# Kernel optimization log

Measured on AMD Instinct MI355X. Metric: run time of the kernel, lower is better.

The kernel has to match this reference:

```python
import jax, jax.numpy as jnp
import numpy as np

B, N, F = 2048, 65536, 128
NUM_K = 3
NUM_LABELS = 10
EXPONENT = 2.0


def setup_inputs() -> dict:
    key = jax.random.key(0)
    k1, k2, k3 = jax.random.split(key, 3)
    # positive inputs: tf.pow with a float exponent NaNs on negative bases
    x_input = jax.random.uniform(k1, (B, F), dtype=jnp.float32)
    train_inputs = jax.random.uniform(k2, (N, F), dtype=jnp.float32)
    train_labels = jax.random.randint(k3, (N,), 0, NUM_LABELS, dtype=jnp.int32)
    features = jnp.ones((F,), dtype=jnp.float32)  # abe_features, ones init
    return {
        "x_input": x_input,
        "train_inputs": train_inputs,
        "train_labels": train_labels,
        "features": features,
    }


def reference(x_input, train_inputs, train_labels, features):
    # weighted_inputs = features * train_inputs
    w = features[None, :] * train_inputs  # [N, F]

    # Minkowsky distance (faithful to the TF graph):
    # (sum(x^p) + sum(w^p))^(1/p) - 2 * x @ w^T
    left = jnp.sum(x_input ** EXPONENT, axis=1)[:, None]   # [B, 1]
    right = jnp.sum(w ** EXPONENT, axis=1)[None, :]        # [1, N]
    distance = (left + right) ** (1.0 / EXPONENT) - 2.0 * (x_input @ w.T)  # [B, N]

    # top-k nearest neighbors via top_k of negated distances
    values, indices = jax.lax.top_k(-distance, NUM_K)      # [B, K]

    # gather neighbor labels and average (tf.reduce_mean on int = floor div)
    labels = train_labels[indices]                          # [B, K] int32
    outputs = jnp.sum(labels, axis=1) // NUM_K              # [B] int32
    one_hot = jax.nn.one_hot(outputs, NUM_LABELS, dtype=jnp.float32)  # [B, NUM_LABELS]

    return (one_hot, values, indices, labels)
```

## Files before the change

### kernel.cpp

```cpp
#include <hip/hip_runtime.h>
#include <hip/hip_bf16.h>
#include <cstdint>
#include <cstddef>

typedef short bf16x8 __attribute__((ext_vector_type(8)));
typedef float f32x4 __attribute__((ext_vector_type(4)));

namespace {
constexpr int kB = 2048;
constexpr int kN = 65536;
constexpr int kF = 128;
constexpr int kLabels = 10;
constexpr int kIMax = 0x7fffffff;

constexpr int BM = 256;
constexpr int BN = 256;
constexpr int SLICE = 2048;
constexpr int NTILES = SLICE / BN;
constexpr int NCH = 12;
constexpr int NCHT = NTILES * NCH;
constexpr int NSUB = kN / 32;
constexpr float kMargin = 0.05f;
}

#define TOP3_INSERT(dd, ii, D0, I0, D1, I1, D2, I2)                              \
  do {                                                                           \
    float _d = (dd); int _i = (ii);                                              \
    if (_d < (D0) || (_d == (D0) && _i < (I0))) {                                \
      (D2) = (D1); (I2) = (I1); (D1) = (D0); (I1) = (I0); (D0) = _d; (I0) = _i;  \
    } else if (_d < (D1) || (_d == (D1) && _i < (I1))) {                         \
      (D2) = (D1); (I2) = (I1); (D1) = _d; (I1) = _i;                            \
    } else if (_d < (D2) || (_d == (D2) && _i < (I2))) {                         \
      (D2) = _d; (I2) = _i;                                                      \
    }                                                                            \
  } while (0)

__device__ inline unsigned short f2bf(float a) {
  __hip_bfloat16 h = __float2bfloat16(a);
  return __builtin_bit_cast(unsigned short, h);
}
__device__ inline float bf2f(unsigned short u) {
  return __bfloat162float(__builtin_bit_cast(__hip_bfloat16, u));
}

__device__ inline void gload_lds16(const void* g, void* l) {
  __builtin_amdgcn_global_load_lds(
      (const __attribute__((address_space(1))) void*)g,
      (__attribute__((address_space(3))) void*)l, 16, 0, 0);
}

__global__ __launch_bounds__(256) void pack_sumsq_kernel(
    const float* __restrict__ x, const float* __restrict__ train,
    const float* __restrict__ features, unsigned short* __restrict__ Ap,
    unsigned short* __restrict__ Bp, float* __restrict__ left,
    float* __restrict__ right) {
  const int wid = (int)((blockIdx.x * 256 + threadIdx.x) >> 6);
  const int lane = threadIdx.x & 63;
  if (wid >= kB + kN) return;
  const float2 fv = reinterpret_cast<const float2*>(features)[lane];
  const float* src;
  unsigned short* dst;
  float pm0, pm1, sm0, sm1;
  if (wid < kB) {
    src = x + (size_t)wid * kF;
    dst = Ap + (size_t)wid * 256;
    pm0 = fv.x; pm1 = fv.y;
    sm0 = 1.0f; sm1 = 1.0f;
  } else {
    src = train + (size_t)(wid - kB) * kF;
    dst = Bp + (size_t)(wid - kB) * 256;
    pm0 = 1.0f; pm1 = 1.0f;
    sm0 = fv.x; sm1 = fv.y;
  }
  const float2 v = reinterpret_cast<const float2*>(src)[lane];
  const float pa = v.x * pm0, pb = v.y * pm1;
  const float sa = v.x * sm0, sb = v.y * sm1;
  const unsigned short ha = f2bf(pa), hb = f2bf(pb);
  const unsigned short la = f2bf(pa - bf2f(ha)), lb = f2bf(pb - bf2f(hb));
  reinterpret_cast<unsigned int*>(dst)[lane] = (unsigned int)ha | ((unsigned int)hb << 16);
  reinterpret_cast<unsigned int*>(dst + 128)[lane] = (unsigned int)la | ((unsigned int)lb << 16);
  float s = sa * sa + sb * sb;
  #pragma unroll
  for (int m = 1; m <= 32; m <<= 1) s += __shfl_xor(s, m);
  if (lane == 0) {
    if (wid < kB) left[wid] = s;
    else right[wid - kB] = s;
  }
}

__global__ __launch_bounds__(512, 2) void knn_main_kernel(
    const unsigned short* __restrict__ Ap, const unsigned short* __restrict__ Bp,
    const float* __restrict__ left, const float* __restrict__ right,
    float* __restrict__ minbuf) {
  __shared__ alignas(16) unsigned short lsA[4][BM * 32];
  __shared__ alignas(16) unsigned short lsB[4][BN * 32];
  __shared__ alignas(16) float lsR[SLICE];

  const int slice = blockIdx.x;
  const int mb = blockIdx.y;
  const int row0 = mb * BM;
  const int col0 = slice * SLICE;
  const int t = threadIdx.x;
  const int lane = t & 63;
  const int wm = (t >> 6) >> 1;
  const int wn = (t >> 6) & 1;

  reinterpret_cast<float4*>(lsR)[t] =
      reinterpret_cast<const float4*>(right + col0)[t];

  float lrow[4][4];
  #pragma unroll
  for (int mf = 0; mf < 4; ++mf)
    #pragma unroll
    for (int rg = 0; rg < 4; ++rg)
      lrow[mf][rg] = left[row0 + wm * 64 + mf * 16 + (lane >> 4) * 4 + rg];

  const int rA = t >> 2;
  const int p = t & 3;
  size_t gbaseA[2], gbaseB[2];
  int ldsoff[2];
  #pragma unroll
  for (int i = 0; i < 2; ++i) {
    const int r = i * 128 + rA;
    const int ps = p ^ ((r >> 1) & 3);
    gbaseA[i] = (size_t)(row0 + r) * 512 + (size_t)ps * 16;
    gbaseB[i] = (size_t)(col0 + r) * 512 + (size_t)ps * 16;
    ldsoff[i] = i * 8192 + t * 16;
  }

  int offA[4], offB[8];
  #pragma unroll
  for (int mf = 0; mf < 4; ++mf) {
    const int rl = wm * 64 + mf * 16 + (lane & 15);
    offA[mf] = rl * 64 + (((lane >> 4) ^ ((rl >> 1) & 3)) * 16);
  }
  #pragma unroll
  for (int nf = 0; nf < 8; ++nf) {
    const int cl = wn * 128 + nf * 16 + (lane & 15);
    offB[nf] = cl * 64 + (((lane >> 4) ^ ((cl >> 1) & 3)) * 16);
  }

  const char* ApB = (const char*)Ap;
  const char* BpB = (const char*)Bp;

  auto stage = [&](int buf, int c, int nt) {
    const int skA = (c < 4) ? c * 32 : ((c < 8) ? 128 + (c - 4) * 32 : (c - 8) * 32);
    const int skB = (c < 4) ? c * 32 : ((c < 8) ? (c - 4) * 32 : 128 + (c - 8) * 32);
    char* lA = (char*)&lsA[buf][0];
    char* lB = (char*)&lsB[buf][0];
    #pragma unroll
    for (int i = 0; i < 2; ++i) {
      gload_lds16(ApB + gbaseA[i] + (size_t)skA * 2, lA + ldsoff[i]);
      gload_lds16(BpB + gbaseB[i] + (size_t)nt * 131072 + (size_t)skB * 2, lB + ldsoff[i]);
    }
  };

  const bool writer = ((lane >> 2) & 3) == (lane >> 4);

  asm volatile("s_waitcnt vmcnt(0) lgkmcnt(0)" ::: "memory");
  __syncthreads();

  int pn = 0, pc = 0;
  #pragma unroll
  for (int i = 0; i < 3; ++i) {
    stage(i, pc, pn);
    if (++pc == NCH) { pc = 0; ++pn; }
  }

  int g = 0;
  for (int nt = 0; nt < NTILES; ++nt) {
    f32x4 acc[4][8];
    #pragma unroll
    for (int mf = 0; mf < 4; ++mf)
      #pragma unroll
      for (int nf = 0; nf < 8; ++nf)
        acc[mf][nf] = (f32x4){0.f, 0.f, 0.f, 0.f};

    for (int c = 0; c < NCH; ++c, ++g) {
      if (g + 3 < NCHT) {
        stage((g + 3) & 3, pc, pn);
        if (++pc == NCH) { pc = 0; ++pn; }
      }
      {
        const int rem = NCHT - 1 - g;
        if (rem >= 3)      asm volatile("s_waitcnt vmcnt(12)" ::: "memory");
        else if (rem == 2) asm volatile("s_waitcnt vmcnt(8)" ::: "memory");
        else if (rem == 1) asm volatile("s_waitcnt vmcnt(4)" ::: "memory");
        else               asm volatile("s_waitcnt vmcnt(0)" ::: "memory");
      }
      __builtin_amdgcn_s_barrier();
      asm volatile("" ::: "memory");

      const char* lA = (const char*)&lsA[g & 3][0];
      const char* lB = (const char*)&lsB[g & 3][0];
      bf16x8 a[4], b[8];
      #pragma unroll
      for (int mf = 0; mf < 4; ++mf)
        a[mf] = *reinterpret_cast<const bf16x8*>(lA + offA[mf]);
      #pragma unroll
      for (int nf = 0; nf < 8; ++nf)
        b[nf] = *reinterpret_cast<const bf16x8*>(lB + offB[nf]);
      asm volatile("s_waitcnt lgkmcnt(0)" ::: "memory");
      __builtin_amdgcn_sched_barrier(0);
      __builtin_amdgcn_s_setprio(1);
      #pragma unroll
      for (int mf = 0; mf < 4; ++mf)
        #pragma unroll
        for (int nf = 0; nf < 8; ++nf)
          acc[mf][nf] = __builtin_amdgcn_mfma_f32_16x16x32_bf16(
              a[mf], b[nf], acc[mf][nf], 0, 0, 0);
      __builtin_amdgcn_s_setprio(0);
      __builtin_amdgcn_s_barrier();
      asm volatile("" ::: "memory");
    }

    float rj[8];
    #pragma unroll
    for (int nf = 0; nf < 8; ++nf)
      rj[nf] = lsR[nt * 256 + wn * 128 + nf * 16 + (lane & 15)];
    const int subbase = slice * 64 + nt * 8 + wn * 4;
    #pragma unroll
    for (int mf = 0; mf < 4; ++mf) {
      #pragma unroll
      for (int rg = 0; rg < 4; ++rg) {
        const float l = lrow[mf][rg];
        float m0, m1, m2, m3;
        #pragma unroll
        for (int nfp = 0; nfp < 4; ++nfp) {
          float da = sqrtf(l + rj[2 * nfp]) - 2.0f * acc[mf][2 * nfp][rg];
          float db = sqrtf(l + rj[2 * nfp + 1]) - 2.0f * acc[mf][2 * nfp + 1][rg];
          float mm = fminf(da, db);
          mm = fminf(mm, __shfl_xor(mm, 1));
          mm = fminf(mm, __shfl_xor(mm, 2));
          mm = fminf(mm, __shfl_xor(mm, 4));
          mm = fminf(mm, __shfl_xor(mm, 8));
          if (nfp == 0) m0 = mm; else if (nfp == 1) m1 = mm;
          else if (nfp == 2) m2 = mm; else m3 = mm;
        }
        if (writer) {
          const int row = row0 + wm * 64 + mf * 16 + (lane >> 4) * 4 + rg;
          const int nfp = lane & 3;
          const float vv = (nfp == 0) ? m0 : (nfp == 1) ? m1 : (nfp == 2) ? m2 : m3;
          minbuf[(size_t)row * NSUB + subbase + nfp] = vv;
        }
      }
    }
  }
}

__global__ __launch_bounds__(256) void select_rescore_kernel(
    const float* __restrict__ x, const float* __restrict__ train,
    const float* __restrict__ features, const float* __restrict__ left,
    const float* __restrict__ right, const int* __restrict__ labels,
    const float* __restrict__ minbuf, float* __restrict__ out) {
  __shared__ float Xs[4][kF];
  const int t = threadIdx.x;
  if (t < 128) {
    const int rr = t >> 5, q = t & 31;
    float4 xv = reinterpret_cast<const float4*>(
        x + (size_t)(blockIdx.x * 4 + rr) * kF)[q];
    const float4 f = reinterpret_cast<const float4*>(features)[q];
    xv.x *= f.x; xv.y *= f.y; xv.z *= f.z; xv.w *= f.w;
    reinterpret_cast<float4*>(&Xs[rr][0])[q] = xv;
  }
  __syncthreads();
  const int wave = t >> 6, lane = t & 63;
  const int row = blockIdx.x * 4 + wave;
  const float lr = left[row];
  const float* mrow = minbuf + (size_t)row * NSUB;

  float v0 = __builtin_inff(), v1 = v0, v2 = v0;
  #pragma unroll 4
  for (int i = 0; i < NSUB / 64; ++i) {
    const float m = mrow[i * 64 + lane];
    if (m < v0) { v2 = v1; v1 = v0; v0 = m; }
    else if (m < v1) { v2 = v1; v1 = m; }
    else if (m < v2) { v2 = m; }
  }
  #pragma unroll
  for (int msk = 1; msk <= 32; msk <<= 1) {
    const float e0 = __shfl_xor(v0, msk), e1 = __shfl_xor(v1, msk), e2 = __shfl_xor(v2, msk);
    if (e0 < v0) { v2 = v1; v1 = v0; v0 = e0; } else if (e0 < v1) { v2 = v1; v1 = e0; } else if (e0 < v2) v2 = e0;
    if (e1 < v0) { v2 = v1; v1 = v0; v0 = e1; } else if (e1 < v1) { v2 = v1; v1 = e1; } else if (e1 < v2) v2 = e1;
    if (e2 < v0) { v2 = v1; v1 = v0; v0 = e2; } else if (e2 < v1) { v2 = v1; v1 = e2; } else if (e2 < v2) v2 = e2;
  }
  const float tau = v2 + kMargin;

  float d0 = __builtin_inff(), d1 = d0, d2 = d0;
  int i0 = kIMax, i1 = kIMax, i2 = kIMax;
  for (int base = 0; base < NSUB; base += 64) {
    const float m = mrow[base + lane];
    unsigned long long msk = __ballot(m <= tau);
    while (msk) {
      const int bpos = __builtin_ctzll(msk);
      msk &= msk - 1;
      const int sub = base + bpos;
      if (lane < 32) {
        const int j = sub * 32 + lane;
        const float4* wp = reinterpret_cast<const float4*>(train + (size_t)j * kF);
        float acc = 0.f;
        #pragma unroll 8
        for (int kq = 0; kq < 32; ++kq) {
          const float4 w4 = wp[kq];
          const float4 x4 = reinterpret_cast<const float4*>(&Xs[wave][0])[kq];
          acc = fmaf(x4.w, w4.w, fmaf(x4.z, w4.z, fmaf(x4.y, w4.y, fmaf(x4.x, w4.x, acc))));
        }
        const float d = sqrtf(lr + right[j]) - 2.0f * acc;
        TOP3_INSERT(d, j, d0, i0, d1, i1, d2, i2);
      }
    }
  }
  #pragma unroll
  for (int msk = 1; msk <= 32; msk <<= 1) {
    const float e0 = __shfl_xor(d0, msk), e1 = __shfl_xor(d1, msk), e2 = __shfl_xor(d2, msk);
    const int f0 = __shfl_xor(i0, msk), f1 = __shfl_xor(i1, msk), f2 = __shfl_xor(i2, msk);
    TOP3_INSERT(e0, f0, d0, i0, d1, i1, d2, i2);
    TOP3_INSERT(e1, f1, d0, i0, d1, i1, d2, i2);
    TOP3_INSERT(e2, f2, d0, i0, d1, i1, d2, i2);
  }
  if (lane == 0) {
    const int l0 = labels[i0], l1 = labels[i1], l2 = labels[i2];
    const int o = (l0 + l1 + l2) / 3;
    float* one_hot = out;
    float* values = out + (size_t)kB * kLabels;
    float* indices = values + (size_t)kB * 3;
    float* labs = indices + (size_t)kB * 3;
    #pragma unroll
    for (int c = 0; c < kLabels; ++c)
      one_hot[(size_t)row * kLabels + c] = (c == o) ? 1.0f : 0.0f;
    values[row * 3 + 0] = -d0; values[row * 3 + 1] = -d1; values[row * 3 + 2] = -d2;
    indices[row * 3 + 0] = (float)i0; indices[row * 3 + 1] = (float)i1; indices[row * 3 + 2] = (float)i2;
    labs[row * 3 + 0] = (float)l0; labs[row * 3 + 1] = (float)l1; labs[row * 3 + 2] = (float)l2;
  }
}

extern "C" void kernel_launch(void* const* d_in, const int* in_sizes, int n_in,
                              void* d_out, int out_size, void* d_ws, size_t ws_size,
                              hipStream_t stream) {
  const float* x = (const float*)d_in[0];
  const float* train = (const float*)d_in[1];
  const int* labels = (const int*)d_in[2];
  const float* features = (const float*)d_in[3];
  float* out = (float*)d_out;

  char* ws = (char*)d_ws;
  unsigned short* Bp = (unsigned short*)ws;
  unsigned short* Ap = (unsigned short*)(ws + 33554432);
  float* left = (float*)(ws + 34603008);
  float* right = (float*)(ws + 34611200);
  float* minbuf = (float*)(ws + 34873344);

  pack_sumsq_kernel<<<((kB + kN) * 64 + 255) / 256, 256, 0, stream>>>(
      x, train, features, Ap, Bp, left, right);
  knn_main_kernel<<<dim3(32, 8), 512, 0, stream>>>(Ap, Bp, left, right, minbuf);
  select_rescore_kernel<<<kB / 4, 256, 0, stream>>>(
      x, train, features, left, right, labels, minbuf, out);
}
```

Measured before the change: 337.7 us.

## Regroup min-bins to cut shuffles in epilogue and drop explicit LDS wait

Each 32-candidate bin is redefined as a strided set of columns: a lane-group's 4 columns across all 8 n-fragments. Most of the min reduction then happens in registers, with only two xor-shuffles instead of sixteen per row. The rescore kernel's index mapping is changed to match the new bin membership. The explicit lgkmcnt wait and sched_barrier before the MFMAs are also removed, letting the compiler interleave LDS reads with MFMA issue. In exchange, the rescore kernel's global reads of training rows become less contiguous.

```diff
diff --git a/kernel.cpp b/kernel.cpp
--- a/kernel.cpp
+++ b/kernel.cpp
@@ -155,8 +155,6 @@
     }
   };
 
-  const bool writer = ((lane >> 2) & 3) == (lane >> 4);
-
   asm volatile("s_waitcnt vmcnt(0) lgkmcnt(0)" ::: "memory");
   __syncthreads();
 
@@ -166,6 +164,8 @@
     stage(i, pc, pn);
     if (++pc == NCH) { pc = 0; ++pn; }
   }
+
+  const bool bwriter = (lane & 3) == 0;
 
   int g = 0;
   for (int nt = 0; nt < NTILES; ++nt) {
@@ -200,8 +200,6 @@
       #pragma unroll
       for (int nf = 0; nf < 8; ++nf)
         b[nf] = *reinterpret_cast<const bf16x8*>(lB + offB[nf]);
-      asm volatile("s_waitcnt lgkmcnt(0)" ::: "memory");
-      __builtin_amdgcn_sched_barrier(0);
       __builtin_amdgcn_s_setprio(1);
       #pragma unroll
       for (int mf = 0; mf < 4; ++mf)
@@ -210,6 +208,7 @@
           acc[mf][nf] = __builtin_amdgcn_mfma_f32_16x16x32_bf16(
               a[mf], b[nf], acc[mf][nf], 0, 0, 0);
       __builtin_amdgcn_s_setprio(0);
+      asm volatile("" ::: "memory");
       __builtin_amdgcn_s_barrier();
       asm volatile("" ::: "memory");
     }
@@ -218,30 +217,25 @@
     #pragma unroll
     for (int nf = 0; nf < 8; ++nf)
       rj[nf] = lsR[nt * 256 + wn * 128 + nf * 16 + (lane & 15)];
-    const int subbase = slice * 64 + nt * 8 + wn * 4;
+    const int binbase = slice * 64 + nt * 8 + wn * 4 + ((lane >> 2) & 3);
     #pragma unroll
     for (int mf = 0; mf < 4; ++mf) {
       #pragma unroll
       for (int rg = 0; rg < 4; ++rg) {
         const float l = lrow[mf][rg];
-        float m0, m1, m2, m3;
+        float d[8];
         #pragma unroll
-        for (int nfp = 0; nfp < 4; ++nfp) {
-          float da = sqrtf(l + rj[2 * nfp]) - 2.0f * acc[mf][2 * nfp][rg];
-          float db = sqrtf(l + rj[2 * nfp + 1]) - 2.0f * acc[mf][2 * nfp + 1][rg];
-          float mm = fminf(da, db);
-          mm = fminf(mm, __shfl_xor(mm, 1));
-          mm = fminf(mm, __shfl_xor(mm, 2));
-          mm = fminf(mm, __shfl_xor(mm, 4));
-          mm = fminf(mm, __shfl_xor(mm, 8));
-          if (nfp == 0) m0 = mm; else if (nfp == 1) m1 = mm;
-          else if (nfp == 2) m2 = mm; else m3 = mm;
-        }
-        if (writer) {
+        for (int nf = 0; nf < 8; ++nf)
+          d[nf] = sqrtf(l + rj[nf]) - 2.0f * acc[mf][nf][rg];
+        d[0] = fminf(d[0], d[4]); d[1] = fminf(d[1], d[5]);
+        d[2] = fminf(d[2], d[6]); d[3] = fminf(d[3], d[7]);
+        d[0] = fminf(d[0], d[2]); d[1] = fminf(d[1], d[3]);
+        float v = fminf(d[0], d[1]);
+        v = fminf(v, __shfl_xor(v, 1));
+        v = fminf(v, __shfl_xor(v, 2));
+        if (bwriter) {
           const int row = row0 + wm * 64 + mf * 16 + (lane >> 4) * 4 + rg;
-          const int nfp = lane & 3;
-          const float vv = (nfp == 0) ? m0 : (nfp == 1) ? m1 : (nfp == 2) ? m2 : m3;
-          minbuf[(size_t)row * NSUB + subbase + nfp] = vv;
+          minbuf[(size_t)row * NSUB + binbase] = v;
         }
       }
     }
@@ -296,7 +290,7 @@
       msk &= msk - 1;
       const int sub = base + bpos;
       if (lane < 32) {
-        const int j = sub * 32 + lane;
+        const int j = (sub >> 2) * 128 + (lane >> 2) * 16 + (sub & 3) * 4 + (lane & 3);
         const float4* wp = reinterpret_cast<const float4*>(train + (size_t)j * kF);
         float acc = 0.f;
         #pragma unroll 8
```

After: 299.2 us. -11.4%, faster.
